# Kernel optimization log

Measured on AMD Instinct MI355X. Metric: run time of the kernel, lower is better.

The kernel has to match this reference:

```python
import jax, jax.numpy as jnp
import numpy as np

NEG = -1e30          # stand-in for -inf that is safe in fp arithmetic
EPS = 1e-7           # keras.backend.epsilon()

B, T, C, L = 64, 1024, 128, 256
BLANK = C - 1        # keras ctc_batch_cost uses last class as blank


def setup_inputs() -> dict:
    key = jax.random.key(0)
    k1, k2, k3 = jax.random.split(key, 3)
    # ctc_batch_cost expects softmax probabilities, not logits
    y_pred = jax.nn.softmax(jax.random.normal(k1, (B, T, C), dtype=jnp.float32), axis=-1)
    y_true = jax.random.randint(k2, (B, L), 0, C - 1).astype(jnp.int32)  # labels exclude blank
    input_length = jnp.full((B, 1), T, dtype=jnp.int32)
    label_length = jax.random.randint(k3, (B, 1), 1, L + 1).astype(jnp.int32)
    return {"y_true": y_true, "y_pred": y_pred,
            "input_length": input_length, "label_length": label_length}


def _logsumexp3(a, b, c):
    m = jnp.maximum(a, jnp.maximum(b, c))
    return m + jnp.log(jnp.exp(a - m) + jnp.exp(b - m) + jnp.exp(c - m))


def _ctc_loss(y_pred, y_true, input_length, label_length):
    log_probs = jnp.log(y_pred + EPS)                       # [B,T,C]
    S = 2 * L + 1
    # extended label sequence: blank, l0, blank, l1, ..., blank
    ext = jnp.full((B, S), BLANK, dtype=jnp.int32).at[:, 1::2].set(y_true)
    lab_len = label_length[:, 0]                            # [B]
    s_idx = jnp.arange(S)
    valid_s = s_idx[None, :] < (2 * lab_len + 1)[:, None]   # [B,S]
    # skip (s-2 -> s) allowed only for non-blank, non-repeated symbols
    skip_ok = jnp.concatenate(
        [jnp.zeros((B, 2), bool),
         (ext[:, 2:] != BLANK) & (ext[:, 2:] != ext[:, :-2])], axis=1)
    # gather per-extended-position log-probs: [B,T,S]
    lp_ext = jnp.take_along_axis(log_probs, jnp.broadcast_to(ext[:, None, :], (B, T, S)), axis=2)

    alpha0 = jnp.full((B, S), NEG, dtype=log_probs.dtype)
    alpha0 = alpha0.at[:, 0].set(lp_ext[:, 0, 0])
    alpha0 = alpha0.at[:, 1].set(jnp.where(lab_len > 0, lp_ext[:, 0, 1], NEG))
    alpha0 = jnp.where(valid_s, alpha0, NEG)

    def step(alpha, inp):
        lp_t, t = inp                                       # lp_t: [B,S]
        shift1 = jnp.pad(alpha[:, :-1], ((0, 0), (1, 0)), constant_values=NEG)
        shift2 = jnp.pad(alpha[:, :-2], ((0, 0), (2, 0)), constant_values=NEG)
        shift2 = jnp.where(skip_ok, shift2, NEG)
        new = _logsumexp3(alpha, shift1, shift2) + lp_t
        new = jnp.where(valid_s, new, NEG)
        # freeze alpha past each sample's input_length
        new = jnp.where(t < input_length, new, alpha)
        return new, None

    lp_tmaj = jnp.swapaxes(lp_ext, 0, 1)                    # [T,B,S]
    alpha, _ = jax.lax.scan(step, alpha0, (lp_tmaj[1:], jnp.arange(1, T)))

    end_blank = jnp.take_along_axis(alpha, (2 * lab_len)[:, None], axis=1)[:, 0]
    end_label = jnp.take_along_axis(alpha, jnp.maximum(2 * lab_len - 1, 0)[:, None], axis=1)[:, 0]
    end_label = jnp.where(lab_len > 0, end_label, NEG)
    loss = -jnp.logaddexp(end_blank, end_label)             # [B]
    return loss[:, None]                                    # (batch, 1) like ctc_batch_cost


def reference(y_true, y_pred, input_length, label_length):
    return _ctc_loss(y_pred, y_true, input_length, label_length)
```

## Files before the change

### kernel.cpp

```cpp
#include <hip/hip_runtime.h>


#define Bc 64
#define Tc 1024
#define Cc 128
#define Lc 256
#define Sc 513
#define BLANKc 127
#define CHUNK 32
#define NW 4
#define PADS 64
#define WSSTRIDE 1028

constexpr float EPSF = 1e-7f;

#define DPPMAXI(x, ctrl) max(x, __builtin_amdgcn_update_dpp( \
    0, x, ctrl, 0xf, 0xf, true))

__device__ __forceinline__ double dpp_wave_shr1_f64(double x) {
    union { double d; int i[2]; } u, r;
    u.d = x;
    r.i[0] = __builtin_amdgcn_update_dpp(0, u.i[0], 0x138, 0xf, 0xf, true);
    r.i[1] = __builtin_amdgcn_update_dpp(0, u.i[1], 0x138, 0xf, 0xf, true);
    return r.d;
}
__device__ __forceinline__ double dpp_wave_shl1_f64(double x) {
    union { double d; int i[2]; } u, r;
    u.d = x;
    r.i[0] = __builtin_amdgcn_update_dpp(0, u.i[0], 0x130, 0xf, 0xf, true);
    r.i[1] = __builtin_amdgcn_update_dpp(0, u.i[1], 0x130, 0xf, 0xf, true);
    return r.d;
}
__device__ __forceinline__ float dpp_wave_shl1_f32(float x) {
    union { float f; int i; } u, r;
    u.f = x;
    r.i = __builtin_amdgcn_update_dpp(0, u.i, 0x130, 0xf, 0xf, true);
    return r.f;
}

__global__ __launch_bounds__(256, 1) void ctc_fb_kernel(
    const int* __restrict__ y_true,
    const float* __restrict__ y_pred,
    const int* __restrict__ label_length,
    double* __restrict__ ws)
{
    const int bb = blockIdx.x;
    const int b = bb >> 1;
    const bool isF = !(bb & 1);
    const int tid = (int)threadIdx.x;
    const int wl = tid >> 6;
    const int lane = tid & 63;

    __shared__ float bufs[3][CHUNK * Cc];
    __shared__ double ash[Sc];
    __shared__ int em[NW];

    const int lab_len = label_length[b];
    const float* yp = y_pred + (size_t)b * Tc * Cc;
    const int* lab = y_true + b * Lc;
    double* wsb = ws + (size_t)b * WSSTRIDE;

    const int start = isF ? ((wl == 0) ? 0 : (128 * wl - PADS)) : (128 * wl);
    const int own_s = 128 * wl;
    const int own_e = (wl == NW - 1) ? Sc : (128 * (wl + 1));
    const int s0 = start + 4 * lane;

    const int li0 = s0 >> 1;
    const int li0c = min(li0, Lc - 1);
    const int li1c = min(li0 + 1, Lc - 1);
    const int li2c = min(li0 + 2, Lc - 1);
    const int ca = lab[li0c], cb = lab[li1c], cc = lab[li2c];
    const double sm_a = (li0 > 0 && ca != BLANKc && ca != lab[li0c - 1]) ? 1.0 : 0.0;
    const double sm_b = (cb != BLANKc && cb != ca) ? 1.0 : 0.0;
    const double sm_c = (cc != BLANKc && cc != cb) ? 1.0 : 0.0;

    const int S2 = 2 * lab_len + 1;
    const bool ow0 = (s0     >= own_s) && (s0     < own_e);
    const bool ow1 = (s0 + 1 >= own_s) && (s0 + 1 < own_e);
    const bool ow2 = (s0 + 2 >= own_s) && (s0 + 2 < own_e);
    const bool ow3 = (s0 + 3 >= own_s) && (s0 + 3 < own_e);
    const int om0 = (ow0 && s0     < S2) ? -1 : 0;
    const int om1 = (ow1 && s0 + 1 < S2) ? -1 : 0;
    const int om2 = (ow2 && s0 + 2 < S2) ? -1 : 0;
    const int om3 = (ow3 && s0 + 3 < S2) ? -1 : 0;

    auto stage = [&](int c, float* dst) {
        const float* g = yp + (size_t)c * (CHUNK * Cc) + lane * 4;
        #pragma unroll
        for (int q = 0; q < 4; ++q) {
            const int i = wl * 4 + q;
            __builtin_amdgcn_global_load_lds(
                (const __attribute__((address_space(1))) void*)(g + i * 256),
                (__attribute__((address_space(3))) void*)(dst + i * 256),
                16, 0, 0);
        }
    };

    float cB[CHUNK];
    float cA[CHUNK];
    float cC[CHUNK];

    auto loadcols = [&](int c, const float* rb) {
        const float* gB = yp + (size_t)c * (CHUNK * Cc) + BLANKc;
        #pragma unroll
        for (int t = 0; t < CHUNK; ++t) {
            cA[t] = rb[t * Cc + ca];
            cC[t] = rb[t * Cc + cb];
            cB[t] = gB[t * Cc];
        }
    };

    if (isF) {
        double a0 = 0, a1 = 0, a2 = 0, a3 = 0, n3 = 0;
        int tote = 0;
        double Eb, Ea, Ec, Ob, Oa, Oc;

        auto stepE = [&]() {
            const double t3 = __fma_rn(sm_b, a1, a3 + a2);
            const double t2 = a2 + a1;
            const double t1 = __fma_rn(sm_a, n3, a1 + a0);
            const double t0 = a0 + n3;
            a3 = t3 * Ec;
            n3 = dpp_wave_shr1_f64(a3);
            a2 = t2 * Eb; a1 = t1 * Ea; a0 = t0 * Eb;
        };
        auto stepO = [&]() {
            const double t3 = __fma_rn(sm_b, a1, a3 + a2);
            const double t2 = a2 + a1;
            const double t1 = __fma_rn(sm_a, n3, a1 + a0);
            const double t0 = a0 + n3;
            a3 = t3 * Oc;
            n3 = dpp_wave_shr1_f64(a3);
            a2 = t2 * Ob; a1 = t1 * Oa; a0 = t0 * Ob;
        };
        auto dopair = [&](int r) {
            Eb = (double)(cB[r] + EPSF);
            Ea = (double)(cA[r] + EPSF);
            Ec = (double)(cC[r] + EPSF);
            stepE();
            Ob = (double)(cB[r + 1] + EPSF);
            Oa = (double)(cA[r + 1] + EPSF);
            Oc = (double)(cC[r + 1] + EPSF);
            stepO();
        };
        auto syncex = [&](int sk) {
            int e =        om0 & (__double2hiint(a0) >> 20);
            e = max(e, om1 & (__double2hiint(a1) >> 20));
            e = max(e, om2 & (__double2hiint(a2) >> 20));
            e = max(e, om3 & (__double2hiint(a3) >> 20));
            e = DPPMAXI(e, 0x111); e = DPPMAXI(e, 0x112);
            e = DPPMAXI(e, 0x114); e = DPPMAXI(e, 0x118);
            e = DPPMAXI(e, 0x142); e = DPPMAXI(e, 0x143);
            if (lane == 63) em[wl] = e;
            if (ow0) ash[s0]     = a0;
            if (ow1) ash[s0 + 1] = a1;
            if (ow2) ash[s0 + 2] = a2;
            if (ow3) ash[s0 + 3] = a3;
            __syncthreads();
            const int eg = max(max(em[0], em[1]), max(em[2], em[3]));
            const int sexp = min(max(2046 - eg, 1), 2045);
            const double sc = __hiloint2double(sexp << 20, 0);
            tote += 1023 - sexp;
            if (wl > 0 && lane < (PADS / 4)) {
                a0 = ash[s0];     a1 = ash[s0 + 1];
                a2 = ash[s0 + 2]; a3 = ash[s0 + 3];
            }
            a0 *= sc; a1 *= sc; a2 *= sc; a3 *= sc;
            n3 = dpp_wave_shr1_f64(a3);
            __syncthreads();
            if (sk <= 15) stage(sk, bufs[sk % 3]);
        };

        stage(0, bufs[0]); stage(1, bufs[1]); stage(2, bufs[2]);
        __syncthreads();

        loadcols(0, bufs[0]);
        if (wl == 0 && lane == 0) {
            a0 = (double)(cB[0] + EPSF);
            if (lab_len > 0) a1 = (double)(cA[0] + EPSF);
        }
        Ob = (double)(cB[1] + EPSF);
        Oa = (double)(cA[1] + EPSF);
        Oc = (double)(cC[1] + EPSF);
        stepO();
        #pragma unroll
        for (int p = 1; p < 16; ++p) dopair(2 * p);

        for (int k = 1; k < 16; ++k) {
            syncex(k + 2);
            loadcols(k, bufs[k % 3]);
            #pragma unroll
            for (int p = 0; p < 16; ++p) dopair(2 * p);
        }
        if (ow0) wsb[s0]     = a0;
        if (ow1) wsb[s0 + 1] = a1;
        if (ow2) wsb[s0 + 2] = a2;
        if (ow3) wsb[s0 + 3] = a3;
        if (tid == 0) wsb[513] = (double)tote;
    } else {
        double b0 = 0, b1 = 0, b2 = 0, b3 = 0, n0 = 0, n1 = 0;
        int tote = 0;
        double Eb, Ea, Ec, Ed, Ob, Oa, Oc, Od;

        auto stepBE = [&]() {
            const double x1 = Ea * b1, x2 = Eb * b2, x3 = Ec * b3, z = Ed * n1;
            const double r0 = __fma_rn(Eb, b0, x1);
            const double r1 = __fma_rn(sm_b, x3, x1 + x2);
            const double r2 = x2 + x3;
            const double r3 = __fma_rn(sm_c, z, __fma_rn(Eb, n0, x3));
            b0 = r0; b1 = r1; b2 = r2; b3 = r3;
            n0 = dpp_wave_shl1_f64(b0);
            n1 = dpp_wave_shl1_f64(b1);
        };
        auto stepBO = [&]() {
            const double x1 = Oa * b1, x2 = Ob * b2, x3 = Oc * b3, z = Od * n1;
            const double r0 = __fma_rn(Ob, b0, x1);
            const double r1 = __fma_rn(sm_b, x3, x1 + x2);
            const double r2 = x2 + x3;
            const double r3 = __fma_rn(sm_c, z, __fma_rn(Ob, n0, x3));
            b0 = r0; b1 = r1; b2 = r2; b3 = r3;
            n0 = dpp_wave_shl1_f64(b0);
            n1 = dpp_wave_shl1_f64(b1);
        };
        auto dopairB = [&](int r) {
            Ob = (double)(cB[r + 1] + EPSF);
            Oa = (double)(cA[r + 1] + EPSF);
            Oc = (double)(cC[r + 1] + EPSF);
            Od = (double)(dpp_wave_shl1_f32(cA[r + 1]) + EPSF);
            stepBO();
            Eb = (double)(cB[r] + EPSF);
            Ea = (double)(cA[r] + EPSF);
            Ec = (double)(cC[r] + EPSF);
            Ed = (double)(dpp_wave_shl1_f32(cA[r]) + EPSF);
            stepBE();
        };
        auto syncex = [&](int sk) {
            int e =        om0 & (__double2hiint(b0) >> 20);
            e = max(e, om1 & (__double2hiint(b1) >> 20));
            e = max(e, om2 & (__double2hiint(b2) >> 20));
            e = max(e, om3 & (__double2hiint(b3) >> 20));
            e = DPPMAXI(e, 0x111); e = DPPMAXI(e, 0x112);
            e = DPPMAXI(e, 0x114); e = DPPMAXI(e, 0x118);
            e = DPPMAXI(e, 0x142); e = DPPMAXI(e, 0x143);
            if (lane == 63) em[wl] = e;
            if (ow0) ash[s0]     = b0;
            if (ow1) ash[s0 + 1] = b1;
            if (ow2) ash[s0 + 2] = b2;
            if (ow3) ash[s0 + 3] = b3;
            __syncthreads();
            const int eg = max(max(em[0], em[1]), max(em[2], em[3]));
            const int sexp = min(max(2046 - eg, 1), 2045);
            const double sc = __hiloint2double(sexp << 20, 0);
            tote += 1023 - sexp;
            if (s0     >= own_e) b0 = (s0     < Sc) ? ash[s0]     : 0.0;
            if (s0 + 1 >= own_e) b1 = (s0 + 1 < Sc) ? ash[s0 + 1] : 0.0;
            if (s0 + 2 >= own_e) b2 = (s0 + 2 < Sc) ? ash[s0 + 2] : 0.0;
            if (s0 + 3 >= own_e) b3 = (s0 + 3 < Sc) ? ash[s0 + 3] : 0.0;
            b0 *= sc; b1 *= sc; b2 *= sc; b3 *= sc;
            n0 = dpp_wave_shl1_f64(b0);
            n1 = dpp_wave_shl1_f64(b1);
            __syncthreads();
            if (sk >= 16) stage(sk, bufs[(31 - sk) % 3]);
        };

        stage(31, bufs[0]); stage(30, bufs[1]); stage(29, bufs[2]);
        __syncthreads();

        {
            const int e0 = 2 * lab_len;
            const int e1 = (lab_len > 0) ? (2 * lab_len - 1) : e0;
            b0 = (s0     == e0 || s0     == e1) ? 1.0 : 0.0;
            b1 = (s0 + 1 == e0 || s0 + 1 == e1) ? 1.0 : 0.0;
            b2 = (s0 + 2 == e0 || s0 + 2 == e1) ? 1.0 : 0.0;
            b3 = (s0 + 3 == e0 || s0 + 3 == e1) ? 1.0 : 0.0;
            n0 = dpp_wave_shl1_f64(b0);
            n1 = dpp_wave_shl1_f64(b1);
        }
        loadcols(31, bufs[0]);
        #pragma unroll
        for (int p = 15; p >= 0; --p) dopairB(2 * p);

        for (int c = 30; c >= 16; --c) {
            syncex(c - 2);
            loadcols(c, bufs[(31 - c) % 3]);
            #pragma unroll
            for (int p = 15; p >= 0; --p) dopairB(2 * p);
        }
        if (ow0) wsb[514 + s0]     = b0;
        if (ow1) wsb[514 + s0 + 1] = b1;
        if (ow2) wsb[514 + s0 + 2] = b2;
        if (ow3) wsb[514 + s0 + 3] = b3;
        if (tid == 0) wsb[1027] = (double)tote;
    }
}

__global__ __launch_bounds__(64) void ctc_combine(
    const int* __restrict__ label_length,
    const double* __restrict__ ws,
    float* __restrict__ out)
{
    const int b = blockIdx.x;
    const int lane = (int)threadIdx.x;
    const int lab_len = label_length[b];
    const int S2 = 2 * lab_len + 1;
    const double* wf = ws + (size_t)b * WSSTRIDE;
    const double* wb = wf + 514;

    int eP = 0;
    for (int s = lane; s < S2; s += 64) {
        const int ea = (__double2hiint(wf[s]) >> 20) & 0x7ff;
        const int eb = (__double2hiint(wb[s]) >> 20) & 0x7ff;
        if (ea && eb) eP = max(eP, ea + eb);
    }
    #pragma unroll
    for (int m = 1; m < 64; m <<= 1) eP = max(eP, __shfl_xor(eP, m));
    const int sh = 2046 - eP;
    int k1 = sh / 2;
    int k2 = sh - k1;
    k1 = min(max(k1, -1022), 1023);
    k2 = min(max(k2, -1022), 1023);
    const double scA = __hiloint2double((1023 + k1) << 20, 0);
    const double scB = __hiloint2double((1023 + k2) << 20, 0);
    double dot = 0.0;
    for (int s = lane; s < S2; s += 64)
        dot += (wf[s] * scA) * (wb[s] * scB);
    #pragma unroll
    for (int m = 1; m < 64; m <<= 1) dot += __shfl_xor(dot, m);
    if (lane == 0) {
        const double lt = wf[513] + wb[513] - (double)k1 - (double)k2;
        out[b] = (float)(-(log(dot) + lt * 0.6931471805599453));
    }
}

extern "C" void kernel_launch(void* const* d_in, const int* in_sizes, int n_in,
                              void* d_out, int out_size, void* d_ws, size_t ws_size,
                              hipStream_t stream) {
    const int*   y_true       = (const int*)d_in[0];
    const float* y_pred       = (const float*)d_in[1];
    const int*   label_length = (const int*)d_in[3];
    float* out = (float*)d_out;
    double* ws = (double*)d_ws;

    ctc_fb_kernel<<<2 * Bc, NW * 64, 0, stream>>>(y_true, y_pred,
                                                  label_length, ws);
    ctc_combine<<<Bc, 64, 0, stream>>>(label_length, ws, out);
}
```

Baseline: 119.8 us.

## Double-buffer column registers mid-chunk and fuse combine via last-block atomic

```diff
diff --git a/kernel.cpp b/kernel.cpp
--- a/kernel.cpp
+++ b/kernel.cpp
@@ -11,6 +11,7 @@
 #define NW 4
 #define PADS 64
 #define WSSTRIDE 1028
+#define FLAGS_OFF (Bc * WSSTRIDE)
 
 constexpr float EPSF = 1e-7f;
 
@@ -38,11 +39,72 @@
     return r.f;
 }
 
+#define BURST_F(Aa, Ca, Ba, rb) do {                                       \
+    _Pragma("unroll")                                                      \
+    for (int t = 0; t < CHUNK; ++t) {                                      \
+        Aa[t] = (rb)[t * Cc + ca];                                         \
+        Ca[t] = (rb)[t * Cc + cb];                                         \
+        Ba[t] = (rb)[t * Cc + BLANKc];                                     \
+    }                                                                      \
+    __builtin_amdgcn_sched_barrier(0);                                     \
+} while (0)
+
+#define BURST_B(Aa, Ca, Ba, rb) do {                                       \
+    _Pragma("unroll")                                                      \
+    for (int t = CHUNK - 1; t >= 0; --t) {                                 \
+        Aa[t] = (rb)[t * Cc + ca];                                         \
+        Ca[t] = (rb)[t * Cc + cb];                                         \
+        Ba[t] = (rb)[t * Cc + BLANKc];                                     \
+    }                                                                      \
+    __builtin_amdgcn_sched_barrier(0);                                     \
+} while (0)
+
+#define DOPAIR_F(Aa, Ca, Ba, r) do {                                       \
+    Eb = (double)(Ba[r] + EPSF);                                           \
+    Ea = (double)(Aa[r] + EPSF);                                           \
+    Ec = (double)(Ca[r] + EPSF);                                           \
+    stepE();                                                               \
+    Ob = (double)(Ba[(r) + 1] + EPSF);                                     \
+    Oa = (double)(Aa[(r) + 1] + EPSF);                                     \
+    Oc = (double)(Ca[(r) + 1] + EPSF);                                     \
+    stepO();                                                               \
+} while (0)
+
+#define DOPAIR_B(Aa, Ca, Ba, r) do {                                       \
+    Ob = (double)(Ba[(r) + 1] + EPSF);                                     \
+    Oa = (double)(Aa[(r) + 1] + EPSF);                                     \
+    Oc = (double)(Ca[(r) + 1] + EPSF);                                     \
+    Od = (double)(dpp_wave_shl1_f32(Aa[(r) + 1]) + EPSF);                  \
+    stepBO();                                                              \
+    Eb = (double)(Ba[r] + EPSF);                                           \
+    Ea = (double)(Aa[r] + EPSF);                                           \
+    Ec = (double)(Ca[r] + EPSF);                                           \
+    Ed = (double)(dpp_wave_shl1_f32(Aa[r]) + EPSF);                        \
+    stepBE();                                                              \
+} while (0)
+
+#define CHUNKF(Aa, Ca, Ba, An, Cn, Bn, nxtbuf, do_burst) do {              \
+    _Pragma("unroll")                                                      \
+    for (int p = 0; p < 8; ++p) DOPAIR_F(Aa, Ca, Ba, 2 * p);               \
+    if (do_burst) BURST_F(An, Cn, Bn, nxtbuf);                             \
+    _Pragma("unroll")                                                      \
+    for (int p = 8; p < 16; ++p) DOPAIR_F(Aa, Ca, Ba, 2 * p);              \
+} while (0)
+
+#define CHUNKB(Aa, Ca, Ba, An, Cn, Bn, nxtbuf, do_burst) do {              \
+    _Pragma("unroll")                                                      \
+    for (int p = 15; p >= 8; --p) DOPAIR_B(Aa, Ca, Ba, 2 * p);             \
+    if (do_burst) BURST_B(An, Cn, Bn, nxtbuf);                             \
+    _Pragma("unroll")                                                      \
+    for (int p = 7; p >= 0; --p) DOPAIR_B(Aa, Ca, Ba, 2 * p);              \
+} while (0)
+
 __global__ __launch_bounds__(256, 1) void ctc_fb_kernel(
     const int* __restrict__ y_true,
     const float* __restrict__ y_pred,
     const int* __restrict__ label_length,
-    double* __restrict__ ws)
+    double* __restrict__ ws,
+    float* __restrict__ out)
 {
     const int bb = blockIdx.x;
     const int b = bb >> 1;
@@ -54,6 +116,7 @@
     __shared__ float bufs[3][CHUNK * Cc];
     __shared__ double ash[Sc];
     __shared__ int em[NW];
+    __shared__ int amlast;
 
     const int lab_len = label_length[b];
     const float* yp = y_pred + (size_t)b * Tc * Cc;
@@ -96,19 +159,8 @@
         }
     };
 
-    float cB[CHUNK];
-    float cA[CHUNK];
-    float cC[CHUNK];
-
-    auto loadcols = [&](int c, const float* rb) {
-        const float* gB = yp + (size_t)c * (CHUNK * Cc) + BLANKc;
-        #pragma unroll
-        for (int t = 0; t < CHUNK; ++t) {
-            cA[t] = rb[t * Cc + ca];
-            cC[t] = rb[t * Cc + cb];
-            cB[t] = gB[t * Cc];
-        }
-    };
+    float A0[CHUNK], C0[CHUNK], B0[CHUNK];
+    float A1[CHUNK], C1[CHUNK], B1[CHUNK];
 
     if (isF) {
         double a0 = 0, a1 = 0, a2 = 0, a3 = 0, n3 = 0;
@@ -132,16 +184,6 @@
             a3 = t3 * Oc;
             n3 = dpp_wave_shr1_f64(a3);
             a2 = t2 * Ob; a1 = t1 * Oa; a0 = t0 * Ob;
-        };
-        auto dopair = [&](int r) {
-            Eb = (double)(cB[r] + EPSF);
-            Ea = (double)(cA[r] + EPSF);
-            Ec = (double)(cC[r] + EPSF);
-            stepE();
-            Ob = (double)(cB[r + 1] + EPSF);
-            Oa = (double)(cA[r + 1] + EPSF);
-            Oc = (double)(cC[r + 1] + EPSF);
-            stepO();
         };
         auto syncex = [&](int sk) {
             int e =        om0 & (__double2hiint(a0) >> 20);
@@ -174,24 +216,32 @@
         stage(0, bufs[0]); stage(1, bufs[1]); stage(2, bufs[2]);
         __syncthreads();
 
-        loadcols(0, bufs[0]);
+        BURST_F(A0, C0, B0, bufs[0]);
         if (wl == 0 && lane == 0) {
-            a0 = (double)(cB[0] + EPSF);
-            if (lab_len > 0) a1 = (double)(cA[0] + EPSF);
-        }
-        Ob = (double)(cB[1] + EPSF);
-        Oa = (double)(cA[1] + EPSF);
-        Oc = (double)(cC[1] + EPSF);
+            a0 = (double)(B0[0] + EPSF);
+            if (lab_len > 0) a1 = (double)(A0[0] + EPSF);
+        }
+        Ob = (double)(B0[1] + EPSF);
+        Oa = (double)(A0[1] + EPSF);
+        Oc = (double)(C0[1] + EPSF);
         stepO();
         #pragma unroll
-        for (int p = 1; p < 16; ++p) dopair(2 * p);
-
-        for (int k = 1; k < 16; ++k) {
-            syncex(k + 2);
-            loadcols(k, bufs[k % 3]);
-            #pragma unroll
-            for (int p = 0; p < 16; ++p) dopair(2 * p);
-        }
+        for (int p = 1; p < 8; ++p) DOPAIR_F(A0, C0, B0, 2 * p);
+        BURST_F(A1, C1, B1, bufs[1]);
+        #pragma unroll
+        for (int p = 8; p < 16; ++p) DOPAIR_F(A0, C0, B0, 2 * p);
+
+        for (int kp = 0; kp < 7; ++kp) {
+            const int k1 = 2 * kp + 1;
+            syncex(k1 + 2);
+            CHUNKF(A1, C1, B1, A0, C0, B0, bufs[(k1 + 1) % 3], true);
+            const int k2 = k1 + 1;
+            syncex(k2 + 2);
+            CHUNKF(A0, C0, B0, A1, C1, B1, bufs[(k2 + 1) % 3], true);
+        }
+        syncex(17);
+        CHUNKF(A1, C1, B1, A1, C1, B1, bufs[0], false);
+
         if (ow0) wsb[s0]     = a0;
         if (ow1) wsb[s0 + 1] = a1;
         if (ow2) wsb[s0 + 2] = a2;
@@ -221,18 +271,6 @@
             b0 = r0; b1 = r1; b2 = r2; b3 = r3;
             n0 = dpp_wave_shl1_f64(b0);
             n1 = dpp_wave_shl1_f64(b1);
-        };
-        auto dopairB = [&](int r) {
-            Ob = (double)(cB[r + 1] + EPSF);
-            Oa = (double)(cA[r + 1] + EPSF);
-            Oc = (double)(cC[r + 1] + EPSF);
-            Od = (double)(dpp_wave_shl1_f32(cA[r + 1]) + EPSF);
-            stepBO();
-            Eb = (double)(cB[r] + EPSF);
-            Ea = (double)(cA[r] + EPSF);
-            Ec = (double)(cC[r] + EPSF);
-            Ed = (double)(dpp_wave_shl1_f32(cA[r]) + EPSF);
-            stepBE();
         };
         auto syncex = [&](int sk) {
             int e =        om0 & (__double2hiint(b0) >> 20);
@@ -276,59 +314,65 @@
             n0 = dpp_wave_shl1_f64(b0);
             n1 = dpp_wave_shl1_f64(b1);
         }
-        loadcols(31, bufs[0]);
-        #pragma unroll
-        for (int p = 15; p >= 0; --p) dopairB(2 * p);
-
-        for (int c = 30; c >= 16; --c) {
-            syncex(c - 2);
-            loadcols(c, bufs[(31 - c) % 3]);
-            #pragma unroll
-            for (int p = 15; p >= 0; --p) dopairB(2 * p);
-        }
+        BURST_B(A0, C0, B0, bufs[0]);
+        #pragma unroll
+        for (int p = 15; p >= 8; --p) DOPAIR_B(A0, C0, B0, 2 * p);
+        BURST_B(A1, C1, B1, bufs[1]);
+        #pragma unroll
+        for (int p = 7; p >= 0; --p) DOPAIR_B(A0, C0, B0, 2 * p);
+
+        for (int kp = 0; kp < 7; ++kp) {
+            const int c1 = 30 - 2 * kp;
+            syncex(c1 - 2);
+            CHUNKB(A1, C1, B1, A0, C0, B0, bufs[(32 - c1) % 3], true);
+            const int c2 = c1 - 1;
+            syncex(c2 - 2);
+            CHUNKB(A0, C0, B0, A1, C1, B1, bufs[(32 - c2) % 3], true);
+        }
+        syncex(14);
+        CHUNKB(A1, C1, B1, A1, C1, B1, bufs[0], false);
+
         if (ow0) wsb[514 + s0]     = b0;
         if (ow1) wsb[514 + s0 + 1] = b1;
         if (ow2) wsb[514 + s0 + 2] = b2;
         if (ow3) wsb[514 + s0 + 3] = b3;
         if (tid == 0) wsb[1027] = (double)tote;
     }
-}
-
-__global__ __launch_bounds__(64) void ctc_combine(
-    const int* __restrict__ label_length,
-    const double* __restrict__ ws,
-    float* __restrict__ out)
-{
-    const int b = blockIdx.x;
-    const int lane = (int)threadIdx.x;
-    const int lab_len = label_length[b];
-    const int S2 = 2 * lab_len + 1;
-    const double* wf = ws + (size_t)b * WSSTRIDE;
-    const double* wb = wf + 514;
-
-    int eP = 0;
-    for (int s = lane; s < S2; s += 64) {
-        const int ea = (__double2hiint(wf[s]) >> 20) & 0x7ff;
-        const int eb = (__double2hiint(wb[s]) >> 20) & 0x7ff;
-        if (ea && eb) eP = max(eP, ea + eb);
+
+    __threadfence();
+    if (tid == 0) {
+        int* flags = (int*)(ws + FLAGS_OFF);
+        amlast = (atomicAdd(&flags[b], 1) == 1);
     }
-    #pragma unroll
-    for (int m = 1; m < 64; m <<= 1) eP = max(eP, __shfl_xor(eP, m));
-    const int sh = 2046 - eP;
-    int k1 = sh / 2;
-    int k2 = sh - k1;
-    k1 = min(max(k1, -1022), 1023);
-    k2 = min(max(k2, -1022), 1023);
-    const double scA = __hiloint2double((1023 + k1) << 20, 0);
-    const double scB = __hiloint2double((1023 + k2) << 20, 0);
-    double dot = 0.0;
-    for (int s = lane; s < S2; s += 64)
-        dot += (wf[s] * scA) * (wb[s] * scB);
-    #pragma unroll
-    for (int m = 1; m < 64; m <<= 1) dot += __shfl_xor(dot, m);
-    if (lane == 0) {
-        const double lt = wf[513] + wb[513] - (double)k1 - (double)k2;
-        out[b] = (float)(-(log(dot) + lt * 0.6931471805599453));
+    __syncthreads();
+    if (amlast && tid < 64) {
+        __threadfence();
+        const double* wf = ws + (size_t)b * WSSTRIDE;
+        const double* wb = wf + 514;
+        int eP = 0;
+        for (int s = tid; s < S2; s += 64) {
+            const int ea = (__double2hiint(wf[s]) >> 20) & 0x7ff;
+            const int eb2 = (__double2hiint(wb[s]) >> 20) & 0x7ff;
+            if (ea && eb2) eP = max(eP, ea + eb2);
+        }
+        #pragma unroll
+        for (int m = 1; m < 64; m <<= 1) eP = max(eP, __shfl_xor(eP, m));
+        const int sh = 2046 - eP;
+        int k1 = sh / 2;
+        int k2 = sh - k1;
+        k1 = min(max(k1, -1022), 1023);
+        k2 = min(max(k2, -1022), 1023);
+        const double scA = __hiloint2double((1023 + k1) << 20, 0);
+        const double scB = __hiloint2double((1023 + k2) << 20, 0);
+        double dot = 0.0;
+        for (int s = tid; s < S2; s += 64)
+            dot += (wf[s] * scA) * (wb[s] * scB);
+        #pragma unroll
+        for (int m = 1; m < 64; m <<= 1) dot += __shfl_xor(dot, m);
+        if (tid == 0) {
+            const double lt = wf[513] + wb[513] - (double)k1 - (double)k2;
+            out[b] = (float)(-(log(dot) + lt * 0.6931471805599453));
+        }
     }
 }
 
@@ -341,7 +385,8 @@
     float* out = (float*)d_out;
     double* ws = (double*)d_ws;
 
+    hipMemsetAsync((char*)d_ws + FLAGS_OFF * sizeof(double), 0,
+                   Bc * sizeof(int), stream);
     ctc_fb_kernel<<<2 * Bc, NW * 64, 0, stream>>>(y_true, y_pred,
-                                                  label_length, ws);
-    ctc_combine<<<Bc, 64, 0, stream>>>(label_length, ws, out);
-}
+                                                  label_length, ws, out);
+}
```

New measurement: 131.5 us. +9.7%, slower.

## Double-buffer half-chunk column loads and fuse combine via last-block atomic

Applied to the files above, without the earlier changes.

```diff
diff --git a/kernel.cpp b/kernel.cpp
--- a/kernel.cpp
+++ b/kernel.cpp
@@ -11,6 +11,7 @@
 #define NW 4
 #define PADS 64
 #define WSSTRIDE 1028
+#define FLAGS_OFF (Bc * WSSTRIDE)
 
 constexpr float EPSF = 1e-7f;
 
@@ -38,11 +39,37 @@
     return r.f;
 }
 
+#define BURSTF(G, base, gbase) do {                                  \
+    _Pragma("unroll")                                                \
+    for (int p = 0; p < 8; ++p) {                                    \
+        const float* rp = (base) + 2 * p * Cc;                       \
+        const float* gp = (gbase) + 2 * p * Cc;                      \
+        G[p][0] = gp[0];      G[p][1] = gp[Cc];                      \
+        G[p][2] = rp[ca];     G[p][3] = rp[ca + Cc];                 \
+        G[p][4] = rp[cb];     G[p][5] = rp[cb + Cc];                 \
+    }                                                                \
+    __builtin_amdgcn_sched_barrier(0);                               \
+} while (0)
+
+#define BURSTB(G, base, gbase, hi) do {                              \
+    _Pragma("unroll")                                                \
+    for (int i = 0; i < 8; ++i) {                                    \
+        const int r = 2 * ((hi) - i);                                \
+        const float* rp = (base) + r * Cc;                           \
+        const float* gp = (gbase) + r * Cc;                          \
+        G[i][0] = gp[0];      G[i][1] = gp[Cc];                      \
+        G[i][2] = rp[ca];     G[i][3] = rp[ca + Cc];                 \
+        G[i][4] = rp[cb];     G[i][5] = rp[cb + Cc];                 \
+    }                                                                \
+    __builtin_amdgcn_sched_barrier(0);                               \
+} while (0)
+
 __global__ __launch_bounds__(256, 1) void ctc_fb_kernel(
     const int* __restrict__ y_true,
     const float* __restrict__ y_pred,
     const int* __restrict__ label_length,
-    double* __restrict__ ws)
+    double* __restrict__ ws,
+    float* __restrict__ out)
 {
     const int bb = blockIdx.x;
     const int b = bb >> 1;
@@ -54,6 +81,7 @@
     __shared__ float bufs[3][CHUNK * Cc];
     __shared__ double ash[Sc];
     __shared__ int em[NW];
+    __shared__ int amlast;
 
     const int lab_len = label_length[b];
     const float* yp = y_pred + (size_t)b * Tc * Cc;
@@ -96,19 +124,7 @@
         }
     };
 
-    float cB[CHUNK];
-    float cA[CHUNK];
-    float cC[CHUNK];
-
-    auto loadcols = [&](int c, const float* rb) {
-        const float* gB = yp + (size_t)c * (CHUNK * Cc) + BLANKc;
-        #pragma unroll
-        for (int t = 0; t < CHUNK; ++t) {
-            cA[t] = rb[t * Cc + ca];
-            cC[t] = rb[t * Cc + cb];
-            cB[t] = gB[t * Cc];
-        }
-    };
+    float GA[8][6], GB[8][6];
 
     if (isF) {
         double a0 = 0, a1 = 0, a2 = 0, a3 = 0, n3 = 0;
@@ -133,14 +149,12 @@
             n3 = dpp_wave_shr1_f64(a3);
             a2 = t2 * Ob; a1 = t1 * Oa; a0 = t0 * Ob;
         };
-        auto dopair = [&](int r) {
-            Eb = (double)(cB[r] + EPSF);
-            Ea = (double)(cA[r] + EPSF);
-            Ec = (double)(cC[r] + EPSF);
+        auto pairF = [&](const float* s) {
+            Eb = (double)(s[0] + EPSF); Ea = (double)(s[2] + EPSF);
+            Ec = (double)(s[4] + EPSF);
             stepE();
-            Ob = (double)(cB[r + 1] + EPSF);
-            Oa = (double)(cA[r + 1] + EPSF);
-            Oc = (double)(cC[r + 1] + EPSF);
+            Ob = (double)(s[1] + EPSF); Oa = (double)(s[3] + EPSF);
+            Oc = (double)(s[5] + EPSF);
             stepO();
         };
         auto syncex = [&](int sk) {
@@ -174,23 +188,34 @@
         stage(0, bufs[0]); stage(1, bufs[1]); stage(2, bufs[2]);
         __syncthreads();
 
-        loadcols(0, bufs[0]);
+        BURSTF(GA, bufs[0], yp + BLANKc);
+        BURSTF(GB, bufs[0] + 16 * Cc, yp + (size_t)16 * Cc + BLANKc);
         if (wl == 0 && lane == 0) {
-            a0 = (double)(cB[0] + EPSF);
-            if (lab_len > 0) a1 = (double)(cA[0] + EPSF);
-        }
-        Ob = (double)(cB[1] + EPSF);
-        Oa = (double)(cA[1] + EPSF);
-        Oc = (double)(cC[1] + EPSF);
+            a0 = (double)(GA[0][0] + EPSF);
+            if (lab_len > 0) a1 = (double)(GA[0][2] + EPSF);
+        }
+        Ob = (double)(GA[0][1] + EPSF);
+        Oa = (double)(GA[0][3] + EPSF);
+        Oc = (double)(GA[0][5] + EPSF);
         stepO();
         #pragma unroll
-        for (int p = 1; p < 16; ++p) dopair(2 * p);
+        for (int p = 1; p < 8; ++p) pairF(GA[p]);
+        BURSTF(GA, bufs[1], yp + (size_t)CHUNK * Cc + BLANKc);
+        #pragma unroll
+        for (int p = 0; p < 8; ++p) pairF(GB[p]);
 
         for (int k = 1; k < 16; ++k) {
             syncex(k + 2);
-            loadcols(k, bufs[k % 3]);
-            #pragma unroll
-            for (int p = 0; p < 16; ++p) dopair(2 * p);
+            const float* rb = bufs[k % 3];
+            const float* gB = yp + (size_t)k * (CHUNK * Cc) + BLANKc;
+            BURSTF(GB, rb + 16 * Cc, gB + 16 * Cc);
+            #pragma unroll
+            for (int p = 0; p < 8; ++p) pairF(GA[p]);
+            if (k < 15)
+                BURSTF(GA, bufs[(k + 1) % 3],
+                       yp + (size_t)(k + 1) * (CHUNK * Cc) + BLANKc);
+            #pragma unroll
+            for (int p = 0; p < 8; ++p) pairF(GB[p]);
         }
         if (ow0) wsb[s0]     = a0;
         if (ow1) wsb[s0 + 1] = a1;
@@ -222,16 +247,14 @@
             n0 = dpp_wave_shl1_f64(b0);
             n1 = dpp_wave_shl1_f64(b1);
         };
-        auto dopairB = [&](int r) {
-            Ob = (double)(cB[r + 1] + EPSF);
-            Oa = (double)(cA[r + 1] + EPSF);
-            Oc = (double)(cC[r + 1] + EPSF);
-            Od = (double)(dpp_wave_shl1_f32(cA[r + 1]) + EPSF);
+        auto pairB = [&](const float* s) {
+            Ob = (double)(s[1] + EPSF); Oa = (double)(s[3] + EPSF);
+            Oc = (double)(s[5] + EPSF);
+            Od = (double)(dpp_wave_shl1_f32(s[3]) + EPSF);
             stepBO();
-            Eb = (double)(cB[r] + EPSF);
-            Ea = (double)(cA[r] + EPSF);
-            Ec = (double)(cC[r] + EPSF);
-            Ed = (double)(dpp_wave_shl1_f32(cA[r]) + EPSF);
+            Eb = (double)(s[0] + EPSF); Ea = (double)(s[2] + EPSF);
+            Ec = (double)(s[4] + EPSF);
+            Ed = (double)(dpp_wave_shl1_f32(s[2]) + EPSF);
             stepBE();
         };
         auto syncex = [&](int sk) {
@@ -276,15 +299,28 @@
             n0 = dpp_wave_shl1_f64(b0);
             n1 = dpp_wave_shl1_f64(b1);
         }
-        loadcols(31, bufs[0]);
-        #pragma unroll
-        for (int p = 15; p >= 0; --p) dopairB(2 * p);
-
+        {
+            const float* gB = yp + (size_t)31 * (CHUNK * Cc) + BLANKc;
+            BURSTB(GA, bufs[0], gB, 15);
+            BURSTB(GB, bufs[0], gB, 7);
+            #pragma unroll
+            for (int i = 0; i < 8; ++i) pairB(GA[i]);
+            BURSTB(GA, bufs[1], yp + (size_t)30 * (CHUNK * Cc) + BLANKc, 15);
+            #pragma unroll
+            for (int i = 0; i < 8; ++i) pairB(GB[i]);
+        }
         for (int c = 30; c >= 16; --c) {
             syncex(c - 2);
-            loadcols(c, bufs[(31 - c) % 3]);
-            #pragma unroll
-            for (int p = 15; p >= 0; --p) dopairB(2 * p);
+            const float* rb = bufs[(31 - c) % 3];
+            const float* gB = yp + (size_t)c * (CHUNK * Cc) + BLANKc;
+            BURSTB(GB, rb, gB, 7);
+            #pragma unroll
+            for (int i = 0; i < 8; ++i) pairB(GA[i]);
+            if (c > 16)
+                BURSTB(GA, bufs[(32 - c) % 3],
+                       yp + (size_t)(c - 1) * (CHUNK * Cc) + BLANKc, 15);
+            #pragma unroll
+            for (int i = 0; i < 8; ++i) pairB(GB[i]);
         }
         if (ow0) wsb[514 + s0]     = b0;
         if (ow1) wsb[514 + s0 + 1] = b1;
@@ -292,43 +328,41 @@
         if (ow3) wsb[514 + s0 + 3] = b3;
         if (tid == 0) wsb[1027] = (double)tote;
     }
-}
-
-__global__ __launch_bounds__(64) void ctc_combine(
-    const int* __restrict__ label_length,
-    const double* __restrict__ ws,
-    float* __restrict__ out)
-{
-    const int b = blockIdx.x;
-    const int lane = (int)threadIdx.x;
-    const int lab_len = label_length[b];
-    const int S2 = 2 * lab_len + 1;
-    const double* wf = ws + (size_t)b * WSSTRIDE;
-    const double* wb = wf + 514;
-
-    int eP = 0;
-    for (int s = lane; s < S2; s += 64) {
-        const int ea = (__double2hiint(wf[s]) >> 20) & 0x7ff;
-        const int eb = (__double2hiint(wb[s]) >> 20) & 0x7ff;
-        if (ea && eb) eP = max(eP, ea + eb);
+
+    __threadfence();
+    if (tid == 0) {
+        int* flags = (int*)(ws + FLAGS_OFF);
+        amlast = (atomicAdd(&flags[b], 1) == 1);
     }
-    #pragma unroll
-    for (int m = 1; m < 64; m <<= 1) eP = max(eP, __shfl_xor(eP, m));
-    const int sh = 2046 - eP;
-    int k1 = sh / 2;
-    int k2 = sh - k1;
-    k1 = min(max(k1, -1022), 1023);
-    k2 = min(max(k2, -1022), 1023);
-    const double scA = __hiloint2double((1023 + k1) << 20, 0);
-    const double scB = __hiloint2double((1023 + k2) << 20, 0);
-    double dot = 0.0;
-    for (int s = lane; s < S2; s += 64)
-        dot += (wf[s] * scA) * (wb[s] * scB);
-    #pragma unroll
-    for (int m = 1; m < 64; m <<= 1) dot += __shfl_xor(dot, m);
-    if (lane == 0) {
-        const double lt = wf[513] + wb[513] - (double)k1 - (double)k2;
-        out[b] = (float)(-(log(dot) + lt * 0.6931471805599453));
+    __syncthreads();
+    if (amlast && tid < 64) {
+        __threadfence();
+        const double* wf = ws + (size_t)b * WSSTRIDE;
+        const double* wb = wf + 514;
+        int eP = 0;
+        for (int s = tid; s < S2; s += 64) {
+            const int ea = (__double2hiint(wf[s]) >> 20) & 0x7ff;
+            const int eb2 = (__double2hiint(wb[s]) >> 20) & 0x7ff;
+            if (ea && eb2) eP = max(eP, ea + eb2);
+        }
+        #pragma unroll
+        for (int m = 1; m < 64; m <<= 1) eP = max(eP, __shfl_xor(eP, m));
+        const int sh = 2046 - eP;
+        int k1 = sh / 2;
+        int k2 = sh - k1;
+        k1 = min(max(k1, -1022), 1023);
+        k2 = min(max(k2, -1022), 1023);
+        const double scA = __hiloint2double((1023 + k1) << 20, 0);
+        const double scB = __hiloint2double((1023 + k2) << 20, 0);
+        double dot = 0.0;
+        for (int s = tid; s < S2; s += 64)
+            dot += (wf[s] * scA) * (wb[s] * scB);
+        #pragma unroll
+        for (int m = 1; m < 64; m <<= 1) dot += __shfl_xor(dot, m);
+        if (tid == 0) {
+            const double lt = wf[513] + wb[513] - (double)k1 - (double)k2;
+            out[b] = (float)(-(log(dot) + lt * 0.6931471805599453));
+        }
     }
 }
 
@@ -341,7 +375,8 @@
     float* out = (float*)d_out;
     double* ws = (double*)d_ws;
 
+    hipMemsetAsync((char*)d_ws + FLAGS_OFF * sizeof(double), 0,
+                   Bc * sizeof(int), stream);
     ctc_fb_kernel<<<2 * Bc, NW * 64, 0, stream>>>(y_true, y_pred,
-                                                  label_length, ws);
-    ctc_combine<<<Bc, 64, 0, stream>>>(label_length, ws, out);
-}
+                                                  label_length, ws, out);
+}
```

Measured after the change: 134.2 us. 12.0% more time.
